# Optimization experiments

Measured on AMD Instinct MI355X. Metric: run time of the kernel, lower is better.

## Reference

```python
import jax, jax.numpy as jnp
import numpy as np

N_NODES = 100000
N_EDGES = 1600000
N_GRAPHS = 512
NUM_REL = 3


def setup_inputs() -> dict:
    key = jax.random.key(0)
    ks = jax.random.split(key, 16)
    shape_idx = jax.random.randint(ks[0], (N_NODES,), 0, 16)
    color_idx = jax.random.randint(ks[1], (N_NODES,), 0, 8)
    node_feats = jnp.stack([shape_idx, color_idx], axis=1)  # [N,2] int
    edge_index = jax.random.randint(ks[2], (2, N_EDGES), 0, N_NODES)
    edge_type = jax.random.randint(ks[3], (N_EDGES,), 0, NUM_REL)
    batch = jnp.sort(jax.random.randint(ks[4], (N_NODES,), 0, N_GRAPHS))
    s = lambda k, sh: jax.random.normal(k, sh, dtype=jnp.float32) * 0.05
    return {
        'node_feats': node_feats,
        'edge_index': edge_index,
        'edge_type': edge_type,
        'batch': batch,
        'shape_emb': s(ks[5], (16, 8)),
        'color_emb': s(ks[6], (8, 8)),
        'pre_w': s(ks[7], (16, 32)),
        'pre_b': jnp.zeros((32,), jnp.float32),
        'root1': s(ks[8], (32, 64)),
        'rel1': s(ks[9], (NUM_REL, 32, 64)),
        'bias1': jnp.zeros((64,), jnp.float32),
        'root2': s(ks[10], (64, 64)),
        'rel2': s(ks[11], (NUM_REL, 64, 64)),
        'bias2': jnp.zeros((64,), jnp.float32),
        'cls_w': s(ks[12], (64, 10)),
        'cls_b': jnp.zeros((10,), jnp.float32),
    }


def rgcn_conv(x, edge_index, edge_type, root, rel_w, bias):
    # PyG RGCNConv: out_i = x_i @ root + sum_r mean_{j in N_r(i)} x_j @ W_r + bias
    src, dst = edge_index[0], edge_index[1]
    out = x @ root + bias
    xs = x[src]  # [E, in] gathered source features
    for r in range(NUM_REL):
        m = (edge_type == r).astype(x.dtype)  # [E]
        msg = (xs @ rel_w[r]) * m[:, None]  # [E, out]
        agg = jax.ops.segment_sum(msg, dst, num_segments=N_NODES)
        cnt = jax.ops.segment_sum(m, dst, num_segments=N_NODES)
        out = out + agg / jnp.maximum(cnt, 1.0)[:, None]
    return out


def reference(node_feats, edge_index, edge_type, batch, shape_emb, color_emb,
              pre_w, pre_b, root1, rel1, bias1, root2, rel2, bias2, cls_w, cls_b):
    x = jnp.concatenate([shape_emb[node_feats[:, 0]], color_emb[node_feats[:, 1]]], axis=1)  # [N,16]
    x = jax.nn.relu(x @ pre_w + pre_b)  # [N,32]
    x = jax.nn.relu(rgcn_conv(x, edge_index, edge_type, root1, rel1, bias1))  # [N,64]
    x = jax.nn.relu(rgcn_conv(x, edge_index, edge_type, root2, rel2, bias2))  # [N,64]
    # global_mean_pool over graph ids
    s = jax.ops.segment_sum(x, batch, num_segments=N_GRAPHS)
    c = jax.ops.segment_sum(jnp.ones((x.shape[0],), x.dtype), batch, num_segments=N_GRAPHS)
    pooled = s / jnp.maximum(c, 1.0)[:, None]  # [G,64]
    return pooled @ cls_w + cls_b  # [G,num_classes]
```

## Files before the change

kernel.cpp:

```cpp
#include <hip/hip_runtime.h>

#define NN 100000
#define NE 1600000
#define NG 512

#define BSH 9
#define NB 196
#define EPB 8192
#define NAB ((NE + EPB - 1) / EPB)
#define CAP 9216

__global__ __launch_bounds__(256) void k_embed(
    const int* __restrict__ nf, const float* __restrict__ semb,
    const float* __restrict__ cemb, const float* __restrict__ pw,
    const float* __restrict__ pb, float* __restrict__ x1)
{
  int gid = blockIdx.x * 256 + threadIdx.x;
  bool valid = gid < NN;
  int i = valid ? gid : NN - 1;
  int sf = nf[2 * i], cf = nf[2 * i + 1];
  float x0[16];
#pragma unroll
  for (int k = 0; k < 8; ++k) x0[k] = semb[sf * 8 + k];
#pragma unroll
  for (int k = 0; k < 8; ++k) x0[8 + k] = cemb[cf * 8 + k];
  float acc[32];
#pragma unroll
  for (int j = 0; j < 32; ++j) acc[j] = pb[j];
#pragma unroll
  for (int k = 0; k < 16; ++k) {
    float xv = x0[k];
#pragma unroll
    for (int j = 0; j < 32; ++j) acc[j] += xv * pw[k * 32 + j];
  }
  if (valid) {
    float4* o = (float4*)(x1 + (size_t)i * 32);
#pragma unroll
    for (int j4 = 0; j4 < 8; ++j4) {
      float4 v;
      v.x = fmaxf(acc[4 * j4 + 0], 0.f);
      v.y = fmaxf(acc[4 * j4 + 1], 0.f);
      v.z = fmaxf(acc[4 * j4 + 2], 0.f);
      v.w = fmaxf(acc[4 * j4 + 3], 0.f);
      o[j4] = v;
    }
  }
}


__global__ __launch_bounds__(256) void kA_count(
    const int* __restrict__ ei, int* __restrict__ bkt_cnt)
{
  __shared__ int lh[NB];
  for (int b = threadIdx.x; b < NB; b += 256) lh[b] = 0;
  __syncthreads();
  int base = blockIdx.x * EPB;
#pragma unroll
  for (int i = 0; i < EPB / 256; ++i) {
    int e = base + i * 256 + threadIdx.x;
    if (e < NE) atomicAdd(&lh[ei[NE + e] >> BSH], 1);
  }
  __syncthreads();
  for (int b = threadIdx.x; b < NB; b += 256)
    if (lh[b]) atomicAdd(&bkt_cnt[b], lh[b]);
}

__global__ __launch_bounds__(256) void kA_scan(
    const int* __restrict__ bkt_cnt, int* __restrict__ bkt_base,
    int* __restrict__ bkt_cur)
{
  __shared__ int sm[2][256];
  int t = threadIdx.x;
  int v = (t < NB) ? bkt_cnt[t] : 0;
  sm[0][t] = v;
  __syncthreads();
  int cur = 0;
#pragma unroll
  for (int off = 1; off < 256; off <<= 1) {
    int add = (t >= off) ? sm[cur][t - off] : 0;
    sm[cur ^ 1][t] = sm[cur][t] + add;
    __syncthreads();
    cur ^= 1;
  }
  if (t < NB) {
    int ex = sm[cur][t] - v;
    bkt_base[t] = ex;
    bkt_cur[t] = ex;
  }
  if (t == 0) bkt_base[NB] = NE;
}

__global__ __launch_bounds__(256) void kA_scatter(
    const int* __restrict__ ei, const int* __restrict__ et,
    int* __restrict__ bkt_cur, int* __restrict__ binned)
{
  __shared__ int packA[EPB];
  __shared__ unsigned char bktA[EPB];
  __shared__ int lh[NB], grun[NB], lcur[NB];
  for (int b = threadIdx.x; b < NB; b += 256) { lh[b] = 0; lcur[b] = 0; }
  __syncthreads();
  int base = blockIdx.x * EPB;
#pragma unroll
  for (int i = 0; i < EPB / 256; ++i) {
    int p = i * 256 + threadIdx.x;
    int e = base + p;
    if (e < NE) {
      int src = ei[e], dst = ei[NE + e], ty = et[e];
      int b = dst >> BSH;
      packA[p] = src | (ty << 17) | ((dst & 511) << 19);
      bktA[p] = (unsigned char)b;
      atomicAdd(&lh[b], 1);
    } else {
      bktA[p] = 255;
    }
  }
  __syncthreads();
  for (int b = threadIdx.x; b < NB; b += 256)
    grun[b] = lh[b] ? atomicAdd(&bkt_cur[b], lh[b]) : 0;
  __syncthreads();
#pragma unroll
  for (int i = 0; i < EPB / 256; ++i) {
    int p = i * 256 + threadIdx.x;
    int b = bktA[p];
    if (b != 255) {
      int off = atomicAdd(&lcur[b], 1);
      binned[grun[b] + off] = packA[p];
    }
  }
}

__global__ __launch_bounds__(512) void kB_build(
    const int* __restrict__ bkt_base, const int* __restrict__ binned,
    int* __restrict__ rs3, int* __restrict__ ep)
{
  __shared__ int stage[CAP];
  __shared__ int ldeg3[1536], lrs3[1536], lcur3[1536];
  __shared__ int sm[2][512];
  int b = blockIdx.x;
  int t = threadIdx.x;
  int p0 = bkt_base[b], p1 = bkt_base[b + 1];
  int cnt = p1 - p0;
  int nodes0 = b << BSH;
  int nnodes = NN - nodes0 < 512 ? NN - nodes0 : 512;
  ldeg3[t] = 0; ldeg3[t + 512] = 0; ldeg3[t + 1024] = 0;
  lcur3[t] = 0; lcur3[t + 512] = 0; lcur3[t + 1024] = 0;
  __syncthreads();
  for (int p = t; p < cnt; p += 512) {
    int pk = binned[p0 + p];
    if (p < CAP) stage[p] = pk;
    int key = ((pk >> 19) & 511) * 3 + ((pk >> 17) & 3);
    atomicAdd(&ldeg3[key], 1);
  }
  __syncthreads();
  int s0 = ldeg3[3 * t], s1 = ldeg3[3 * t + 1], s2 = ldeg3[3 * t + 2];
  int tot = s0 + s1 + s2;
  sm[0][t] = tot;
  __syncthreads();
  int cur = 0;
#pragma unroll
  for (int off = 1; off < 512; off <<= 1) {
    int add = (t >= off) ? sm[cur][t - off] : 0;
    sm[cur ^ 1][t] = sm[cur][t] + add;
    __syncthreads();
    cur ^= 1;
  }
  int ex = sm[cur][t] - tot;
  int r0 = p0 + ex, r1 = r0 + s0, r2 = r1 + s1;
  lrs3[3 * t] = r0;
  lrs3[3 * t + 1] = r1;
  lrs3[3 * t + 2] = r2;
  if (t < nnodes) {
    size_t base3 = (size_t)(nodes0 + t) * 3;
    rs3[base3 + 0] = r0;
    rs3[base3 + 1] = r1;
    rs3[base3 + 2] = r2;
  }
  if (b == NB - 1 && t == 0) rs3[(size_t)NN * 3] = NE;
  __syncthreads();
  for (int p = t; p < cnt; p += 512) {
    int pk = (p < CAP) ? stage[p] : binned[p0 + p];
    int key = ((pk >> 19) & 511) * 3 + ((pk >> 17) & 3);
    int off = atomicAdd(&lcur3[key], 1);
    ep[lrs3[key] + off] = pk & 0x1FFFF;
  }
}

template <int IN>
__global__ __launch_bounds__(256) void k_agg(
    const float* __restrict__ x, const int* __restrict__ rs3,
    const int* __restrict__ ep, float* __restrict__ h)
{
  constexpr int LPE = IN / 4;
  constexpr int DPW = (IN == 32) ? 2 : 1;
  constexpr int SW = 64 / DPW;
  constexpr int EPI = SW / LPE;
  int tid = threadIdx.x;
  int wid = (blockIdx.x * 256 + tid) >> 6;
  int lane = tid & 63;
  int sub = lane / SW;
  int sl = lane % SW;
  int k4 = sl % LPE;
  int es = sl / LPE;
  int d = wid * DPW + sub;
  if (d >= NN) return;
  int q0 = rs3[3 * d + 0];
  int q1 = rs3[3 * d + 1];
  int q2 = rs3[3 * d + 2];
  int q3 = rs3[3 * d + 3];
  float* hd = h + (size_t)d * 3 * IN;
#pragma unroll
  for (int r = 0; r < 3; ++r) {
    int pA = (r == 0) ? q0 : (r == 1) ? q1 : q2;
    int pB = (r == 0) ? q1 : (r == 1) ? q2 : q3;
    float4 a = make_float4(0.f, 0.f, 0.f, 0.f);
    for (int p = pA; p < pB; p += EPI) {
      int idx = p + es;
      bool val = idx < pB;
      int e = ep[val ? idx : pB - 1];
      float4 v = *(const float4*)(x + (size_t)e * IN + k4 * 4);
      if (val) { a.x += v.x; a.y += v.y; a.z += v.z; a.w += v.w; }
    }
#pragma unroll
    for (int off = LPE; off < SW; off <<= 1) {
      a.x += __shfl_xor(a.x, off, 64);
      a.y += __shfl_xor(a.y, off, 64);
      a.z += __shfl_xor(a.z, off, 64);
      a.w += __shfl_xor(a.w, off, 64);
    }
    if (es == 0) {
      float cf = (float)((pB - pA) > 0 ? (pB - pA) : 1);
      float4 o;
      o.x = a.x / cf; o.y = a.y / cf; o.z = a.z / cf; o.w = a.w / cf;
      *(float4*)(hd + r * IN + k4 * 4) = o;
    }
  }
}

template <int IN>
__global__ __launch_bounds__(512) void k_mat(
    const float* __restrict__ x, const float* __restrict__ h,
    const float* __restrict__ root, const float* __restrict__ rel,
    const float* __restrict__ bias, float* __restrict__ y)
{
  __shared__ float smem[3 * IN][65];
  const int tid = threadIdx.x;
  const int node0 = blockIdx.x * 64;
  const int n = tid & 63;
  const int j0 = __builtin_amdgcn_readfirstlane((tid >> 6) * 8);

  constexpr int F4 = IN / 4;
  constexpr int NPF = (64 * F4) / 512;

  for (int idx = tid; idx < 64 * F4; idx += 512) {
    int nn = idx / F4, c4 = idx % F4;
    int node = node0 + nn;
    float4 v = make_float4(0.f, 0.f, 0.f, 0.f);
    if (node < NN) v = *(const float4*)(x + (size_t)node * IN + c4 * 4);
    smem[c4 * 4 + 0][nn] = v.x;
    smem[c4 * 4 + 1][nn] = v.y;
    smem[c4 * 4 + 2][nn] = v.z;
    smem[c4 * 4 + 3][nn] = v.w;
  }
#pragma unroll
  for (int r = 0; r < 2; ++r) {
    for (int idx = tid; idx < 64 * F4; idx += 512) {
      int nn = idx / F4, c4 = idx % F4;
      int node = node0 + nn;
      float4 v = make_float4(0.f, 0.f, 0.f, 0.f);
      if (node < NN) v = *(const float4*)(h + ((size_t)node * 3 + r) * IN + c4 * 4);
      smem[(1 + r) * IN + c4 * 4 + 0][nn] = v.x;
      smem[(1 + r) * IN + c4 * 4 + 1][nn] = v.y;
      smem[(1 + r) * IN + c4 * 4 + 2][nn] = v.z;
      smem[(1 + r) * IN + c4 * 4 + 3][nn] = v.w;
    }
  }
  __syncthreads();

  float4 pf[NPF];
#pragma unroll
  for (int u = 0; u < NPF; ++u) {
    int idx = u * 512 + tid;
    int nn = idx / F4, c4 = idx % F4;
    int node = node0 + nn;
    pf[u] = make_float4(0.f, 0.f, 0.f, 0.f);
    if (node < NN) pf[u] = *(const float4*)(h + ((size_t)node * 3 + 2) * IN + c4 * 4);
  }

  float acc[8];
#pragma unroll
  for (int j = 0; j < 8; ++j) acc[j] = bias[j0 + j];

  auto mm = [&](const float* __restrict__ W, int row0) {
#pragma unroll 4
    for (int k = 0; k < IN; ++k) {
      float sk = smem[row0 + k][n];
      const float* w = W + (size_t)k * 64 + j0;
#pragma unroll
      for (int j = 0; j < 8; ++j) acc[j] = fmaf(sk, w[j], acc[j]);
    }
  };

  mm(root, 0);
  mm(rel, IN);
  mm(rel + (size_t)IN * 64, 2 * IN);
  __syncthreads();

#pragma unroll
  for (int u = 0; u < NPF; ++u) {
    int idx = u * 512 + tid;
    int nn = idx / F4, c4 = idx % F4;
    smem[c4 * 4 + 0][nn] = pf[u].x;
    smem[c4 * 4 + 1][nn] = pf[u].y;
    smem[c4 * 4 + 2][nn] = pf[u].z;
    smem[c4 * 4 + 3][nn] = pf[u].w;
  }
  __syncthreads();
  mm(rel + (size_t)2 * IN * 64, 0);

  int node = node0 + n;
  if (node < NN) {
    float4* o = (float4*)(y + (size_t)node * 64 + j0);
    float4 v;
    v.x = fmaxf(acc[0], 0.f);
    v.y = fmaxf(acc[1], 0.f);
    v.z = fmaxf(acc[2], 0.f);
    v.w = fmaxf(acc[3], 0.f);
    o[0] = v;
    v.x = fmaxf(acc[4], 0.f);
    v.y = fmaxf(acc[5], 0.f);
    v.z = fmaxf(acc[6], 0.f);
    v.w = fmaxf(acc[7], 0.f);
    o[1] = v;
  }
}

__global__ __launch_bounds__(256) void k_pool(
    const float* __restrict__ x3, const int* __restrict__ batch,
    float* __restrict__ pooled, float* __restrict__ gcnt)
{
  int gwave = (blockIdx.x * 256 + threadIdx.x) >> 6;
  int lane = threadIdx.x & 63;
  int n0 = gwave * 64;
  if (n0 >= NN) return;
  int n1 = n0 + 64 < NN ? n0 + 64 : NN;
  int gcur = batch[n0];
  float acc = 0.f;
  int run = 0;
  for (int n = n0; n < n1; ++n) {
    int g = batch[n];
    if (g != gcur) {
      atomicAdd(&pooled[gcur * 64 + lane], acc);
      if (lane == 0) atomicAdd(&gcnt[gcur], (float)run);
      acc = 0.f; run = 0; gcur = g;
    }
    acc += x3[(size_t)n * 64 + lane];
    ++run;
  }
  atomicAdd(&pooled[gcur * 64 + lane], acc);
  if (lane == 0) atomicAdd(&gcnt[gcur], (float)run);
}

__global__ __launch_bounds__(256) void k_cls(
    const float* __restrict__ pooled, const float* __restrict__ gcnt,
    const float* __restrict__ cw, const float* __restrict__ cb, float* __restrict__ out)
{
  int t = blockIdx.x * 256 + threadIdx.x;
  if (t >= NG * 10) return;
  int g = t / 10, c = t % 10;
  float cf = fmaxf(gcnt[g], 1.f);
  float acc = cb[c];
#pragma unroll 8
  for (int k = 0; k < 64; ++k)
    acc += (pooled[g * 64 + k] / cf) * cw[k * 10 + c];
  out[t] = acc;
}

extern "C" void kernel_launch(void* const* d_in, const int* in_sizes, int n_in,
                              void* d_out, int out_size, void* d_ws, size_t ws_size,
                              hipStream_t stream)
{
  const int* nf = (const int*)d_in[0];
  const int* ei = (const int*)d_in[1];
  const int* et = (const int*)d_in[2];
  const int* batch = (const int*)d_in[3];
  const float* semb = (const float*)d_in[4];
  const float* cemb = (const float*)d_in[5];
  const float* pw = (const float*)d_in[6];
  const float* pb = (const float*)d_in[7];
  const float* root1 = (const float*)d_in[8];
  const float* rel1 = (const float*)d_in[9];
  const float* bias1 = (const float*)d_in[10];
  const float* root2 = (const float*)d_in[11];
  const float* rel2 = (const float*)d_in[12];
  const float* bias2 = (const float*)d_in[13];
  const float* cw = (const float*)d_in[14];
  const float* cb = (const float*)d_in[15];
  float* out = (float*)d_out;

  char* ws = (char*)d_ws;
  size_t off = 0;
  auto alloc = [&](size_t bytes) {
    char* p = ws + off;
    off += (bytes + 255) & ~(size_t)255;
    return p;
  };
  int* bkt_cnt = (int*)alloc((size_t)NB * 4);
  int* bkt_base = (int*)alloc((size_t)(NB + 1) * 4);
  int* bkt_cur = (int*)alloc((size_t)NB * 4);
  int* rs3 = (int*)alloc(((size_t)NN * 3 + 1) * 4);
  int* ep = (int*)alloc((size_t)NE * 4 + 256);
  float* xA = (float*)alloc((size_t)NN * 64 * 4);
  float* xB = (float*)alloc((size_t)NN * 64 * 4);
  float* h = (float*)alloc((size_t)3 * NN * 64 * 4);
  float* pooled = (float*)alloc((size_t)NG * 64 * 4);
  float* gcnt = (float*)alloc((size_t)NG * 4);
  int* binned = (int*)h;
  (void)ws_size; (void)in_sizes; (void)n_in; (void)out_size;

  hipMemsetAsync(bkt_cnt, 0, (size_t)NB * 4, stream);
  k_embed<<<(NN + 255) / 256, 256, 0, stream>>>(nf, semb, cemb, pw, pb, xB);

  kA_count<<<NAB, 256, 0, stream>>>(ei, bkt_cnt);
  kA_scan<<<1, 256, 0, stream>>>(bkt_cnt, bkt_base, bkt_cur);
  kA_scatter<<<NAB, 256, 0, stream>>>(ei, et, bkt_cur, binned);
  kB_build<<<NB, 512, 0, stream>>>(bkt_base, binned, rs3, ep);

  int matgrid = (NN + 63) / 64;

  k_agg<32><<<(NN / 2 + 3) / 4 + 1, 256, 0, stream>>>(xB, rs3, ep, h);
  k_mat<32><<<matgrid, 512, 0, stream>>>(xB, h, root1, rel1, bias1, xA);
  k_agg<64><<<(NN + 3) / 4, 256, 0, stream>>>(xA, rs3, ep, h);
  k_mat<64><<<matgrid, 512, 0, stream>>>(xA, h, root2, rel2, bias2, xB);

  hipMemsetAsync(pooled, 0, (size_t)NG * 64 * 4, stream);
  hipMemsetAsync(gcnt, 0, (size_t)NG * 4, stream);
  int nwaves = (NN + 63) / 64;
  k_pool<<<(nwaves + 3) / 4, 256, 0, stream>>>(xB, batch, pooled, gcnt);
  k_cls<<<(NG * 10 + 255) / 256, 256, 0, stream>>>(pooled, gcnt, cw, cb, out);
}
```

Baseline: 329.1 us.

## Transform node features before gathering and fuse mean aggregation with root and ReLU

Reorders each RGCN layer to first compute per-relation transformed features for every node, then gather those per edge with mean weights and fuse the root term, bias and ReLU in the gather kernel. This removes the separate aggregated buffer read by the matmul kernel and merges the three relation loops into one edge loop. In exchange, layer 1 now gathers 64-wide rows instead of 32-wide, and the gathered table is three times larger, which increases random-read traffic.

```diff
diff --git a/kernel.cpp b/kernel.cpp
--- a/kernel.cpp
+++ b/kernel.cpp
@@ -186,70 +186,17 @@
 }
 
 template <int IN>
-__global__ __launch_bounds__(256) void k_agg(
-    const float* __restrict__ x, const int* __restrict__ rs3,
-    const int* __restrict__ ep, float* __restrict__ h)
-{
-  constexpr int LPE = IN / 4;
-  constexpr int DPW = (IN == 32) ? 2 : 1;
-  constexpr int SW = 64 / DPW;
-  constexpr int EPI = SW / LPE;
-  int tid = threadIdx.x;
-  int wid = (blockIdx.x * 256 + tid) >> 6;
-  int lane = tid & 63;
-  int sub = lane / SW;
-  int sl = lane % SW;
-  int k4 = sl % LPE;
-  int es = sl / LPE;
-  int d = wid * DPW + sub;
-  if (d >= NN) return;
-  int q0 = rs3[3 * d + 0];
-  int q1 = rs3[3 * d + 1];
-  int q2 = rs3[3 * d + 2];
-  int q3 = rs3[3 * d + 3];
-  float* hd = h + (size_t)d * 3 * IN;
-#pragma unroll
-  for (int r = 0; r < 3; ++r) {
-    int pA = (r == 0) ? q0 : (r == 1) ? q1 : q2;
-    int pB = (r == 0) ? q1 : (r == 1) ? q2 : q3;
-    float4 a = make_float4(0.f, 0.f, 0.f, 0.f);
-    for (int p = pA; p < pB; p += EPI) {
-      int idx = p + es;
-      bool val = idx < pB;
-      int e = ep[val ? idx : pB - 1];
-      float4 v = *(const float4*)(x + (size_t)e * IN + k4 * 4);
-      if (val) { a.x += v.x; a.y += v.y; a.z += v.z; a.w += v.w; }
-    }
-#pragma unroll
-    for (int off = LPE; off < SW; off <<= 1) {
-      a.x += __shfl_xor(a.x, off, 64);
-      a.y += __shfl_xor(a.y, off, 64);
-      a.z += __shfl_xor(a.z, off, 64);
-      a.w += __shfl_xor(a.w, off, 64);
-    }
-    if (es == 0) {
-      float cf = (float)((pB - pA) > 0 ? (pB - pA) : 1);
-      float4 o;
-      o.x = a.x / cf; o.y = a.y / cf; o.z = a.z / cf; o.w = a.w / cf;
-      *(float4*)(hd + r * IN + k4 * 4) = o;
-    }
-  }
-}
-
-template <int IN>
-__global__ __launch_bounds__(512) void k_mat(
-    const float* __restrict__ x, const float* __restrict__ h,
-    const float* __restrict__ root, const float* __restrict__ rel,
-    const float* __restrict__ bias, float* __restrict__ y)
-{
-  __shared__ float smem[3 * IN][65];
+__global__ __launch_bounds__(512) void k_trans(
+    const float* __restrict__ x, const float* __restrict__ root,
+    const float* __restrict__ rel, const float* __restrict__ bias,
+    float* __restrict__ yrel, float* __restrict__ yroot)
+{
+  __shared__ float smem[IN][65];
   const int tid = threadIdx.x;
   const int node0 = blockIdx.x * 64;
   const int n = tid & 63;
   const int j0 = __builtin_amdgcn_readfirstlane((tid >> 6) * 8);
-
   constexpr int F4 = IN / 4;
-  constexpr int NPF = (64 * F4) / 512;
 
   for (int idx = tid; idx < 64 * F4; idx += 512) {
     int nn = idx / F4, c4 = idx % F4;
@@ -261,76 +208,91 @@
     smem[c4 * 4 + 2][nn] = v.z;
     smem[c4 * 4 + 3][nn] = v.w;
   }
-#pragma unroll
-  for (int r = 0; r < 2; ++r) {
-    for (int idx = tid; idx < 64 * F4; idx += 512) {
-      int nn = idx / F4, c4 = idx % F4;
-      int node = node0 + nn;
-      float4 v = make_float4(0.f, 0.f, 0.f, 0.f);
-      if (node < NN) v = *(const float4*)(h + ((size_t)node * 3 + r) * IN + c4 * 4);
-      smem[(1 + r) * IN + c4 * 4 + 0][nn] = v.x;
-      smem[(1 + r) * IN + c4 * 4 + 1][nn] = v.y;
-      smem[(1 + r) * IN + c4 * 4 + 2][nn] = v.z;
-      smem[(1 + r) * IN + c4 * 4 + 3][nn] = v.w;
-    }
-  }
-  __syncthreads();
-
-  float4 pf[NPF];
-#pragma unroll
-  for (int u = 0; u < NPF; ++u) {
-    int idx = u * 512 + tid;
-    int nn = idx / F4, c4 = idx % F4;
-    int node = node0 + nn;
-    pf[u] = make_float4(0.f, 0.f, 0.f, 0.f);
-    if (node < NN) pf[u] = *(const float4*)(h + ((size_t)node * 3 + 2) * IN + c4 * 4);
-  }
+  __syncthreads();
+
+  const int node = node0 + n;
+  const bool valid = node < NN;
 
   float acc[8];
-#pragma unroll
-  for (int j = 0; j < 8; ++j) acc[j] = bias[j0 + j];
-
-  auto mm = [&](const float* __restrict__ W, int row0) {
+  auto mm = [&](const float* __restrict__ W) {
 #pragma unroll 4
     for (int k = 0; k < IN; ++k) {
-      float sk = smem[row0 + k][n];
+      float sk = smem[k][n];
       const float* w = W + (size_t)k * 64 + j0;
 #pragma unroll
       for (int j = 0; j < 8; ++j) acc[j] = fmaf(sk, w[j], acc[j]);
     }
   };
 
-  mm(root, 0);
-  mm(rel, IN);
-  mm(rel + (size_t)IN * 64, 2 * IN);
-  __syncthreads();
-
-#pragma unroll
-  for (int u = 0; u < NPF; ++u) {
-    int idx = u * 512 + tid;
-    int nn = idx / F4, c4 = idx % F4;
-    smem[c4 * 4 + 0][nn] = pf[u].x;
-    smem[c4 * 4 + 1][nn] = pf[u].y;
-    smem[c4 * 4 + 2][nn] = pf[u].z;
-    smem[c4 * 4 + 3][nn] = pf[u].w;
-  }
-  __syncthreads();
-  mm(rel + (size_t)2 * IN * 64, 0);
-
-  int node = node0 + n;
-  if (node < NN) {
-    float4* o = (float4*)(y + (size_t)node * 64 + j0);
-    float4 v;
-    v.x = fmaxf(acc[0], 0.f);
-    v.y = fmaxf(acc[1], 0.f);
-    v.z = fmaxf(acc[2], 0.f);
-    v.w = fmaxf(acc[3], 0.f);
-    o[0] = v;
-    v.x = fmaxf(acc[4], 0.f);
-    v.y = fmaxf(acc[5], 0.f);
-    v.z = fmaxf(acc[6], 0.f);
-    v.w = fmaxf(acc[7], 0.f);
-    o[1] = v;
+#pragma unroll
+  for (int s = 0; s < 3; ++s) {
+#pragma unroll
+    for (int j = 0; j < 8; ++j) acc[j] = 0.f;
+    mm(rel + (size_t)s * IN * 64);
+    if (valid) {
+      float4* o = (float4*)(yrel + ((size_t)node * 3 + s) * 64 + j0);
+      o[0] = make_float4(acc[0], acc[1], acc[2], acc[3]);
+      o[1] = make_float4(acc[4], acc[5], acc[6], acc[7]);
+    }
+  }
+#pragma unroll
+  for (int j = 0; j < 8; ++j) acc[j] = bias[j0 + j];
+  mm(root);
+  if (valid) {
+    float4* o = (float4*)(yroot + (size_t)node * 64 + j0);
+    o[0] = make_float4(acc[0], acc[1], acc[2], acc[3]);
+    o[1] = make_float4(acc[4], acc[5], acc[6], acc[7]);
+  }
+}
+
+__global__ __launch_bounds__(256) void k_gather(
+    const float* __restrict__ yrel, const float* __restrict__ yroot,
+    const int* __restrict__ rs3, const int* __restrict__ ep,
+    float* __restrict__ xout)
+{
+  int tid = threadIdx.x;
+  int d = (blockIdx.x * 256 + tid) >> 6;
+  int lane = tid & 63;
+  int k4 = lane & 15;
+  int es = lane >> 4;
+  if (d >= NN) return;
+  int q0 = rs3[3 * d + 0];
+  int q1 = rs3[3 * d + 1];
+  int q2 = rs3[3 * d + 2];
+  int q3 = rs3[3 * d + 3];
+  int c0 = q1 - q0, c1 = q2 - q1, c2 = q3 - q2;
+  float w0 = 1.f / (float)(c0 > 0 ? c0 : 1);
+  float w1 = 1.f / (float)(c1 > 0 ? c1 : 1);
+  float w2 = 1.f / (float)(c2 > 0 ? c2 : 1);
+  float4 a = make_float4(0.f, 0.f, 0.f, 0.f);
+#pragma unroll 2
+  for (int p = q0; p < q3; p += 4) {
+    int idx = p + es;
+    bool val = idx < q3;
+    int e = ep[val ? idx : q3 - 1];
+    int r = (idx < q1) ? 0 : ((idx < q2) ? 1 : 2);
+    float w = val ? ((idx < q1) ? w0 : ((idx < q2) ? w1 : w2)) : 0.f;
+    float4 v = *(const float4*)(yrel + ((size_t)e * 3 + r) * 64 + k4 * 4);
+    a.x = fmaf(w, v.x, a.x);
+    a.y = fmaf(w, v.y, a.y);
+    a.z = fmaf(w, v.z, a.z);
+    a.w = fmaf(w, v.w, a.w);
+  }
+#pragma unroll
+  for (int off = 16; off < 64; off <<= 1) {
+    a.x += __shfl_xor(a.x, off, 64);
+    a.y += __shfl_xor(a.y, off, 64);
+    a.z += __shfl_xor(a.z, off, 64);
+    a.w += __shfl_xor(a.w, off, 64);
+  }
+  if (es == 0) {
+    float4 rt = *(const float4*)(yroot + (size_t)d * 64 + k4 * 4);
+    float4 o;
+    o.x = fmaxf(rt.x + a.x, 0.f);
+    o.y = fmaxf(rt.y + a.y, 0.f);
+    o.z = fmaxf(rt.z + a.z, 0.f);
+    o.w = fmaxf(rt.w + a.w, 0.f);
+    *(float4*)(xout + (size_t)d * 64 + k4 * 4) = o;
   }
 }
 
@@ -409,12 +371,13 @@
   int* bkt_cur = (int*)alloc((size_t)NB * 4);
   int* rs3 = (int*)alloc(((size_t)NN * 3 + 1) * 4);
   int* ep = (int*)alloc((size_t)NE * 4 + 256);
+  float* yrel = (float*)alloc((size_t)NN * 3 * 64 * 4);
+  float* yroot = (float*)alloc((size_t)NN * 64 * 4);
   float* xA = (float*)alloc((size_t)NN * 64 * 4);
   float* xB = (float*)alloc((size_t)NN * 64 * 4);
-  float* h = (float*)alloc((size_t)3 * NN * 64 * 4);
   float* pooled = (float*)alloc((size_t)NG * 64 * 4);
   float* gcnt = (float*)alloc((size_t)NG * 4);
-  int* binned = (int*)h;
+  int* binned = (int*)yrel;
   (void)ws_size; (void)in_sizes; (void)n_in; (void)out_size;
 
   hipMemsetAsync(bkt_cnt, 0, (size_t)NB * 4, stream);
@@ -425,12 +388,13 @@
   kA_scatter<<<NAB, 256, 0, stream>>>(ei, et, bkt_cur, binned);
   kB_build<<<NB, 512, 0, stream>>>(bkt_base, binned, rs3, ep);
 
-  int matgrid = (NN + 63) / 64;
-
-  k_agg<32><<<(NN / 2 + 3) / 4 + 1, 256, 0, stream>>>(xB, rs3, ep, h);
-  k_mat<32><<<matgrid, 512, 0, stream>>>(xB, h, root1, rel1, bias1, xA);
-  k_agg<64><<<(NN + 3) / 4, 256, 0, stream>>>(xA, rs3, ep, h);
-  k_mat<64><<<matgrid, 512, 0, stream>>>(xA, h, root2, rel2, bias2, xB);
+  int tgrid = (NN + 63) / 64;
+  int ggrid = (NN + 3) / 4;
+
+  k_trans<32><<<tgrid, 512, 0, stream>>>(xB, root1, rel1, bias1, yrel, yroot);
+  k_gather<<<ggrid, 256, 0, stream>>>(yrel, yroot, rs3, ep, xA);
+  k_trans<64><<<tgrid, 512, 0, stream>>>(xA, root2, rel2, bias2, yrel, yroot);
+  k_gather<<<ggrid, 256, 0, stream>>>(yrel, yroot, rs3, ep, xB);
 
   hipMemsetAsync(pooled, 0, (size_t)NG * 64 * 4, stream);
   hipMemsetAsync(gcnt, 0, (size_t)NG * 4, stream);
```

Result: no change. 332.2 us (+0.9%).
